# Kernel tuning notes

Measured on AMD Instinct MI355X. Metric: run time of the kernel, lower is better.

## Reference

```python
import jax, jax.numpy as jnp
import numpy as np

H, W = 256, 256
S, S_IDX, END_BIAS = 48, 3, 10
E_IDX = S - END_BIAS          # 38
N_ITER = E_IDX - (S_IDX + 1)  # 34 sequential segments after the start segment
OUT_WIN = 10                  # outlier1d window length
OUT_THRESH = 2.0


def setup_inputs() -> dict:
    key = jax.random.key(0)
    # (x, y) event coordinates in [0, W) x [0, H); t/p/b columns are unused by the module.
    events = jax.random.uniform(key, (16, 960000, 2), jnp.float32, minval=0.0, maxval=256.0)
    return {"events": events}


def _blur(a):
    """5x5 uniform (0.04) blur, SAME padding; a: [B, S, D] -> [B, S, D]."""
    k = jnp.full((1, 1, 5, 5), 0.04, jnp.float32)
    return jax.lax.conv_general_dilated(a[:, None], k, (1, 1), [(2, 2), (2, 2)])[:, 0]


def _outlier_flags(m):
    """outlier1d(m[b, si:si+10], thresh=2)[0] for si in [S_IDX+1, E_IDX). m: [B,S] -> bool [B,N_ITER]."""
    widx = (jnp.arange(N_ITER)[:, None] + S_IDX + 1) + jnp.arange(OUT_WIN)[None, :]
    w = m[:, widx]                                   # [B, N_ITER, 10]
    med = jnp.median(w, axis=-1, keepdims=True)
    diff = jnp.abs(w - med)
    mad = jnp.median(diff, axis=-1)                  # [B, N_ITER]
    return 0.6745 * diff[..., 0] / mad > OUT_THRESH


def reference(events):
    B, N, _ = events.shape
    segmentLen = N // S            # static python int
    Nu = segmentLen * S
    x = events[:, :Nu, 0].astype(jnp.int32)   # [B, Nu]
    y = events[:, :Nu, 1].astype(jnp.int32)
    chunks = jnp.repeat(jnp.arange(S), segmentLen)   # segment id per event, [Nu]
    bidx = jnp.arange(B)[:, None]

    # per-batch x-t / y-t histograms via scatter-add
    alongX = jnp.zeros((B, S, W), jnp.float32).at[bidx, chunks[None, :], x].add(1.0)
    alongY = jnp.zeros((B, S, H), jnp.float32).at[bidx, chunks[None, :], y].add(1.0)

    def proc_axis(along, D):
        flat = along.reshape(B, -1)
        cv = (flat.mean(-1) + 3.0 * jnp.std(flat, axis=-1, ddof=1))[:, None, None]
        a = _blur(jnp.clip(along, 0.0, cv))
        m = jnp.einsum('bsd,d->bs', a, jnp.arange(D, dtype=jnp.float32)) / segmentLen
        start = m[:, S_IDX:S_IDX + 1]
        aligned = jnp.round(m - start - (D // 2 - start)).astype(jnp.int32)
        return m, aligned

    meanX, alignedX = proc_axis(alongX, W)
    meanY, alignedY = proc_axis(alongY, H)
    is_out = _outlier_flags(meanX) | _outlier_flags(meanY)   # [B, N_ITER]

    def per_batch(xb, yb, aX, aY, outb):
        xs = jnp.clip(xb - aX[chunks], 0, W - 1)
        ys = jnp.clip(yb - aY[chunks], 0, H - 1)
        idx_c = (xs + W * ys).reshape(S, segmentLen)
        idx_v = (xs // 2 + (W // 2) * (ys // 2)).reshape(S, segmentLen)
        container0 = jnp.zeros(W * H, jnp.int32).at[idx_c[S_IDX]].add(1)
        ver0 = jnp.zeros((W // 2) * (H // 2), bool).at[idx_v[S_IDX]].set(True)

        def step(carry, inp):
            container, ver, stopped = carry
            ic, iv, is_o = inp
            ver_new = ver.at[iv].set(True)
            cnt = jnp.sum(ver_new).astype(jnp.float32)
            new_info = jnp.sum(jnp.logical_xor(ver_new, ver)).astype(jnp.float32)
            brk = new_info / cnt < 0.1
            do = (~stopped) & (~is_o) & (~brk)
            stopped = stopped | ((~stopped) & (~is_o) & brk)
            container = jnp.where(do, container.at[ic].add(1), container)
            ver = jnp.where(do, ver_new, ver)
            return (container, ver, stopped), None

        (container, _, _), _ = jax.lax.scan(
            step, (container0, ver0, jnp.array(False)),
            (idx_c[S_IDX + 1:E_IDX], idx_v[S_IDX + 1:E_IDX], outb))
        c = container.astype(jnp.float32)
        cv = c.mean() + 3.0 * jnp.std(c, ddof=1)
        return jnp.clip(c, 0.0, cv) / cv

    containers = jax.vmap(per_batch)(x, y, alignedX, alignedY, is_out)  # [B, W*H]
    return containers.reshape(B, 1, H, W)
```

## Files before the change

### kernel.cpp

```cpp
#include <hip/hip_runtime.h>

#define NB 16
#define NEV 960000
#define NS 48
#define SEG 20000
#define S_IDX 3
#define E_IDX 38
#define N_ITER 34
#define ND 256
#define NCH 35

__global__ __launch_bounds__(256) void hist_kernel(const float* __restrict__ events,
                                                   float* __restrict__ alongX,
                                                   float* __restrict__ alongY) {
    __shared__ unsigned hx[ND], hy[ND];
    int tid = threadIdx.x;
    int blk = blockIdx.x;
    int b = blk / NS, c = blk % NS;
    hx[tid] = 0; hy[tid] = 0;
    __syncthreads();
    size_t base = (size_t)b * NEV + (size_t)c * SEG;
    const float4* ev4 = (const float4*)(events + base * 2);
    for (int k = tid; k < SEG / 2; k += 256) {
        float4 v = ev4[k];
        int x0 = (int)v.x, y0 = (int)v.y, x1 = (int)v.z, y1 = (int)v.w;
        x0 = x0 > 255 ? 255 : x0; y0 = y0 > 255 ? 255 : y0;
        x1 = x1 > 255 ? 255 : x1; y1 = y1 > 255 ? 255 : y1;
        atomicAdd(&hx[x0], 1u); atomicAdd(&hy[y0], 1u);
        atomicAdd(&hx[x1], 1u); atomicAdd(&hy[y1], 1u);
    }
    __syncthreads();
    int o = (b * NS + c) * ND + tid;
    alongX[o] = (float)hx[tid];
    alongY[o] = (float)hy[tid];
}

__global__ __launch_bounds__(256) void stats_kernel(const float* __restrict__ alongX,
                                                    const float* __restrict__ alongY,
                                                    int* __restrict__ alignedX,
                                                    int* __restrict__ alignedY,
                                                    float* __restrict__ m_all) {
    __shared__ float sbuf[NS * ND];
    __shared__ double sredA[4], sredB[4];
    __shared__ float scv;
    int tid = threadIdx.x;
    int b = blockIdx.x >> 1, axis = blockIdx.x & 1;
    const float* along = (axis ? alongY : alongX) + (size_t)b * NS * ND;
    for (int k = 0; k < NS; k++) sbuf[k * ND + tid] = along[k * ND + tid];
    __syncthreads();
    double s = 0.0, s2 = 0.0;
    for (int k = 0; k < NS; k++) { double v = sbuf[k * ND + tid]; s += v; s2 += v * v; }
    for (int off = 32; off; off >>= 1) { s += __shfl_down(s, off); s2 += __shfl_down(s2, off); }
    if ((tid & 63) == 0) { sredA[tid >> 6] = s; sredB[tid >> 6] = s2; }
    __syncthreads();
    if (tid == 0) {
        double ts = sredA[0] + sredA[1] + sredA[2] + sredA[3];
        double ts2 = sredB[0] + sredB[1] + sredB[2] + sredB[3];
        const double N = (double)(NS * ND);
        double mean = ts / N;
        double var  = (ts2 - ts * ts / N) / (N - 1.0);
        scv = (float)(mean + 3.0 * sqrt(var));
    }
    __syncthreads();
    float cv = scv;
    int wave = tid >> 6, lane = tid & 63;
    for (int q = 0; q < 12; ++q) {
        int sI = wave * 12 + q;
        double acc = 0.0;
        #pragma unroll
        for (int k = 0; k < 4; ++k) {
            int d = lane + 64 * k;
            int lo = d - 2 < 0 ? 0 : d - 2;
            int hi = d + 2 > 255 ? 255 : d + 2;
            double Wd = 0.5 * (double)(lo + hi) * (double)(hi - lo + 1);
            double t = 0.0;
            #pragma unroll
            for (int ds = -2; ds <= 2; ++ds) {
                int ss = sI + ds;
                if (ss >= 0 && ss < NS) t += (double)fminf(sbuf[ss * ND + d], cv);
            }
            acc += t * Wd;
        }
        for (int off = 32; off; off >>= 1) acc += __shfl_down(acc, off);
        if (lane == 0) {
            float mf = (float)(acc * 0.04 / (double)SEG);
            m_all[(b * 2 + axis) * NS + sI] = mf;
            (axis ? alignedY : alignedX)[b * NS + sI] = (int)rintf(mf - 128.0f);
        }
    }
}

__global__ __launch_bounds__(256) void mask_kernel(const float* __restrict__ events,
                                                   const int* __restrict__ alignedX,
                                                   const int* __restrict__ alignedY,
                                                   unsigned* __restrict__ masks) {
    __shared__ unsigned sm[512];
    int tid = threadIdx.x, blk = blockIdx.x;
    int b = blk / NCH, ci = blk % NCH, si = S_IDX + ci;
    sm[tid] = 0; sm[tid + 256] = 0;
    __syncthreads();
    int aX = alignedX[b * NS + si], aY = alignedY[b * NS + si];
    const float4* ev = (const float4*)(events + ((size_t)b * NEV + (size_t)si * SEG) * 2);
    for (int i = tid; i < SEG / 2; i += 256) {
        float4 e = ev[i];
        int xs0 = (int)e.x - aX; xs0 = xs0 < 0 ? 0 : (xs0 > 255 ? 255 : xs0);
        int ys0 = (int)e.y - aY; ys0 = ys0 < 0 ? 0 : (ys0 > 255 ? 255 : ys0);
        int xs1 = (int)e.z - aX; xs1 = xs1 < 0 ? 0 : (xs1 > 255 ? 255 : xs1);
        int ys1 = (int)e.w - aY; ys1 = ys1 < 0 ? 0 : (ys1 > 255 ? 255 : ys1);
        int iv0 = (xs0 >> 1) | ((ys0 >> 1) << 7);
        int iv1 = (xs1 >> 1) | ((ys1 >> 1) << 7);
        atomicOr(&sm[iv0 >> 5], 1u << (iv0 & 31));
        atomicOr(&sm[iv1 >> 5], 1u << (iv1 & 31));
    }
    __syncthreads();
    unsigned* mo = masks + (size_t)blk * 512;
    mo[tid] = sm[tid];
    mo[tid + 256] = sm[tid + 256];
}

__device__ inline float median10(const float* v) {
    float w[10];
    #pragma unroll
    for (int i = 0; i < 10; i++) w[i] = v[i];
    #pragma unroll
    for (int i = 1; i < 10; i++) {
        float k = w[i]; int j = i - 1;
        while (j >= 0 && w[j] > k) { w[j + 1] = w[j]; j--; }
        w[j + 1] = k;
    }
    return 0.5f * (w[4] + w[5]);
}

__device__ inline bool outlier_flag(const float* w) {
    float med = median10(w);
    float d[10];
    #pragma unroll
    for (int i = 0; i < 10; i++) d[i] = fabsf(w[i] - med);
    float d0 = d[0];
    float mad = median10(d);
    return (0.6745f * d0 / mad) > 2.0f;
}

__device__ inline unsigned wave_sum_u32(unsigned v) {
    for (int off = 32; off; off >>= 1) v += __shfl_xor(v, off);
    return v;
}

__global__ __launch_bounds__(64) void decide_kernel(const unsigned* __restrict__ masks,
                                                    const float* __restrict__ m_all,
                                                    unsigned long long* __restrict__ commitmask) {
    int b = blockIdx.x, lane = threadIdx.x;
    bool f = false;
    if (lane < N_ITER) {
        const float* mx = m_all + b * 2 * NS;
        const float* my = mx + NS;
        f = outlier_flag(&mx[S_IDX + 1 + lane]) || outlier_flag(&my[S_IDX + 1 + lane]);
    }
    unsigned long long omask = __ballot(f);
    const unsigned* mb = masks + (size_t)b * NCH * 512;
    uint4 v0 = ((const uint4*)mb)[lane * 2];
    uint4 v1 = ((const uint4*)mb)[lane * 2 + 1];
    unsigned ver[8] = {v0.x, v0.y, v0.z, v0.w, v1.x, v1.y, v1.z, v1.w};
    unsigned pc = 0;
    #pragma unroll
    for (int j = 0; j < 8; j++) pc += __popc(ver[j]);
    unsigned cnt = wave_sum_u32(pc);
    unsigned long long cm = 1ull;
    for (int si = S_IDX + 1; si < E_IDX; ++si) {
        int idx = si - S_IDX;
        const uint4* dp = (const uint4*)(mb + (size_t)idx * 512);
        uint4 d0 = dp[lane * 2], d1 = dp[lane * 2 + 1];
        unsigned del[8] = {d0.x, d0.y, d0.z, d0.w, d1.x, d1.y, d1.z, d1.w};
        unsigned nl = 0;
        #pragma unroll
        for (int j = 0; j < 8; j++) nl += __popc(del[j] & ~ver[j]);
        unsigned ni = wave_sum_u32(nl);
        bool is_o = (omask >> (si - S_IDX - 1)) & 1;
        if (!is_o) {
            unsigned cn = cnt + ni;
            float ratio = (float)ni / (float)cn;
            if (ratio < 0.1f) break;
            cm |= 1ull << idx;
            cnt = cn;
            #pragma unroll
            for (int j = 0; j < 8; j++) ver[j] |= del[j];
        }
    }
    if (lane == 0) commitmask[b] = cm;
}

__global__ __launch_bounds__(256) void commit_kernel(const float* __restrict__ events,
                                                     const int* __restrict__ alignedX,
                                                     const int* __restrict__ alignedY,
                                                     const unsigned long long* __restrict__ commitmask,
                                                     unsigned* __restrict__ container) {
    int blk = blockIdx.x, tid = threadIdx.x;
    int b = blk / NCH, ci = blk % NCH;
    if (!((commitmask[b] >> ci) & 1ull)) return;
    int si = S_IDX + ci;
    int aX = alignedX[b * NS + si], aY = alignedY[b * NS + si];
    unsigned* cont = container + (size_t)b * 65536;
    const float4* ev = (const float4*)(events + ((size_t)b * NEV + (size_t)si * SEG) * 2);
    for (int i = tid; i < SEG / 2; i += 256) {
        float4 e = ev[i];
        int xs0 = (int)e.x - aX; xs0 = xs0 < 0 ? 0 : (xs0 > 255 ? 255 : xs0);
        int ys0 = (int)e.y - aY; ys0 = ys0 < 0 ? 0 : (ys0 > 255 ? 255 : ys0);
        int xs1 = (int)e.z - aX; xs1 = xs1 < 0 ? 0 : (xs1 > 255 ? 255 : xs1);
        int ys1 = (int)e.w - aY; ys1 = ys1 < 0 ? 0 : (ys1 > 255 ? 255 : ys1);
        atomicAdd(&cont[xs0 | (ys0 << 8)], 1u);
        atomicAdd(&cont[xs1 | (ys1 << 8)], 1u);
    }
}

__global__ __launch_bounds__(256) void cv_kernel(const unsigned* __restrict__ container,
                                                 float* __restrict__ cvb) {
    __shared__ double sredA[4], sredB[4];
    int tid = threadIdx.x, b = blockIdx.x;
    const uint4* c4 = (const uint4*)(container + (size_t)b * 65536);
    double s = 0.0, s2 = 0.0;
    for (int i = tid; i < 16384; i += 256) {
        uint4 v = c4[i];
        double a0 = v.x, a1 = v.y, a2 = v.z, a3 = v.w;
        s += a0 + a1 + a2 + a3;
        s2 += a0 * a0 + a1 * a1 + a2 * a2 + a3 * a3;
    }
    for (int off = 32; off; off >>= 1) { s += __shfl_down(s, off); s2 += __shfl_down(s2, off); }
    if ((tid & 63) == 0) { sredA[tid >> 6] = s; sredB[tid >> 6] = s2; }
    __syncthreads();
    if (tid == 0) {
        double ts = sredA[0] + sredA[1] + sredA[2] + sredA[3];
        double ts2 = sredB[0] + sredB[1] + sredB[2] + sredB[3];
        double mean = ts / 65536.0;
        double var = (ts2 - ts * ts / 65536.0) / 65535.0;
        cvb[b] = (float)(mean + 3.0 * sqrt(var));
    }
}

__global__ __launch_bounds__(256) void finish_kernel(const unsigned* __restrict__ container,
                                                     const float* __restrict__ cvb,
                                                     float* __restrict__ out) {
    int g = blockIdx.x * 256 + threadIdx.x;
    int b = g >> 14;
    float cv = cvb[b];
    uint4 v = ((const uint4*)container)[g];
    float4 o;
    o.x = fminf((float)v.x, cv) / cv;
    o.y = fminf((float)v.y, cv) / cv;
    o.z = fminf((float)v.z, cv) / cv;
    o.w = fminf((float)v.w, cv) / cv;
    ((float4*)out)[g] = o;
}

extern "C" void kernel_launch(void* const* d_in, const int* in_sizes, int n_in,
                              void* d_out, int out_size, void* d_ws, size_t ws_size,
                              hipStream_t stream) {
    const float* events = (const float*)d_in[0];
    float* out = (float*)d_out;
    char* ws = (char*)d_ws;

    float*    alongX    = (float*)(ws);
    float*    alongY    = (float*)(ws + 786432);
    unsigned* masks     = (unsigned*)(ws);
    unsigned* container = (unsigned*)(ws + 1572864);
    int*      alignedX  = (int*)(ws + 5767168);
    int*      alignedY  = (int*)(ws + 5770240);
    float*    m_all     = (float*)(ws + 5773312);
    unsigned long long* commitmask = (unsigned long long*)(ws + 5779456);
    float*    cvb       = (float*)(ws + 5779584);

    hipMemsetAsync(container, 0, (size_t)NB * 65536 * sizeof(unsigned), stream);
    hist_kernel<<<NB * NS, 256, 0, stream>>>(events, alongX, alongY);
    stats_kernel<<<NB * 2, 256, 0, stream>>>(alongX, alongY, alignedX, alignedY, m_all);
    mask_kernel<<<NB * NCH, 256, 0, stream>>>(events, alignedX, alignedY, masks);
    decide_kernel<<<NB, 64, 0, stream>>>(masks, m_all, commitmask);
    commit_kernel<<<NB * NCH, 256, 0, stream>>>(events, alignedX, alignedY, commitmask, container);
    cv_kernel<<<NB, 256, 0, stream>>>(container, cvb);
    finish_kernel<<<1024, 256, 0, stream>>>(container, cvb, out);
}
```

Measured before the change: 307.2 us.

## Compact events to packed 16-bit coords in hist pass; fold container memset in

The histogram kernel now also writes each event of segments 3..37 as a packed pair of 8-bit x/y coordinates, two events per 32-bit word. The mask and commit kernels read this compact buffer instead of re-reading the float events, which cuts their global read traffic by a factor of four. The container zeroing moves into the histogram kernel, removing the separate memset. The cost is an extra write of about 22 MB in the histogram pass. A stub commit_kernel is left behind unused.

```diff
diff --git a/kernel.cpp b/kernel.cpp
--- a/kernel.cpp
+++ b/kernel.cpp
@@ -12,15 +12,24 @@
 
 __global__ __launch_bounds__(256) void hist_kernel(const float* __restrict__ events,
                                                    float* __restrict__ alongX,
-                                                   float* __restrict__ alongY) {
+                                                   float* __restrict__ alongY,
+                                                   unsigned* __restrict__ compact,
+                                                   unsigned* __restrict__ container) {
     __shared__ unsigned hx[ND], hy[ND];
     int tid = threadIdx.x;
     int blk = blockIdx.x;
     int b = blk / NS, c = blk % NS;
     hx[tid] = 0; hy[tid] = 0;
+    {
+        uint4 z = {0u, 0u, 0u, 0u};
+        for (int i = blk * 256 + tid; i < 262144; i += NB * NS * 256)
+            ((uint4*)container)[i] = z;
+    }
     __syncthreads();
     size_t base = (size_t)b * NEV + (size_t)c * SEG;
     const float4* ev4 = (const float4*)(events + base * 2);
+    bool wr = (c >= S_IDX && c < E_IDX);
+    unsigned* dst = wr ? compact + ((size_t)b * NCH + (c - S_IDX)) * (SEG / 2) : nullptr;
     for (int k = tid; k < SEG / 2; k += 256) {
         float4 v = ev4[k];
         int x0 = (int)v.x, y0 = (int)v.y, x1 = (int)v.z, y1 = (int)v.w;
@@ -28,6 +37,7 @@
         x1 = x1 > 255 ? 255 : x1; y1 = y1 > 255 ? 255 : y1;
         atomicAdd(&hx[x0], 1u); atomicAdd(&hy[y0], 1u);
         atomicAdd(&hx[x1], 1u); atomicAdd(&hy[y1], 1u);
+        if (wr) dst[k] = (unsigned)(x0 | (y0 << 8)) | ((unsigned)(x1 | (y1 << 8)) << 16);
     }
     __syncthreads();
     int o = (b * NS + c) * ND + tid;
@@ -90,7 +100,7 @@
     }
 }
 
-__global__ __launch_bounds__(256) void mask_kernel(const float* __restrict__ events,
+__global__ __launch_bounds__(256) void mask_kernel(const unsigned* __restrict__ compact,
                                                    const int* __restrict__ alignedX,
                                                    const int* __restrict__ alignedY,
                                                    unsigned* __restrict__ masks) {
@@ -100,17 +110,22 @@
     sm[tid] = 0; sm[tid + 256] = 0;
     __syncthreads();
     int aX = alignedX[b * NS + si], aY = alignedY[b * NS + si];
-    const float4* ev = (const float4*)(events + ((size_t)b * NEV + (size_t)si * SEG) * 2);
-    for (int i = tid; i < SEG / 2; i += 256) {
-        float4 e = ev[i];
-        int xs0 = (int)e.x - aX; xs0 = xs0 < 0 ? 0 : (xs0 > 255 ? 255 : xs0);
-        int ys0 = (int)e.y - aY; ys0 = ys0 < 0 ? 0 : (ys0 > 255 ? 255 : ys0);
-        int xs1 = (int)e.z - aX; xs1 = xs1 < 0 ? 0 : (xs1 > 255 ? 255 : xs1);
-        int ys1 = (int)e.w - aY; ys1 = ys1 < 0 ? 0 : (ys1 > 255 ? 255 : ys1);
-        int iv0 = (xs0 >> 1) | ((ys0 >> 1) << 7);
-        int iv1 = (xs1 >> 1) | ((ys1 >> 1) << 7);
-        atomicOr(&sm[iv0 >> 5], 1u << (iv0 & 31));
-        atomicOr(&sm[iv1 >> 5], 1u << (iv1 & 31));
+    const uint4* cp = (const uint4*)(compact + ((size_t)b * NCH + ci) * (SEG / 2));
+    for (int i = tid; i < SEG / 8; i += 256) {
+        uint4 w = cp[i];
+        unsigned ws[4] = {w.x, w.y, w.z, w.w};
+        #pragma unroll
+        for (int j = 0; j < 4; j++) {
+            unsigned v = ws[j];
+            #pragma unroll
+            for (int h = 0; h < 2; h++) {
+                unsigned e = (h ? (v >> 16) : v) & 0xFFFFu;
+                int xs = (int)(e & 255u) - aX; xs = xs < 0 ? 0 : (xs > 255 ? 255 : xs);
+                int ys = (int)(e >> 8)   - aY; ys = ys < 0 ? 0 : (ys > 255 ? 255 : ys);
+                int iv = (xs >> 1) | ((ys >> 1) << 7);
+                atomicOr(&sm[iv >> 5], 1u << (iv & 31));
+            }
+        }
     }
     __syncthreads();
     unsigned* mo = masks + (size_t)blk * 512;
@@ -189,26 +204,42 @@
     if (lane == 0) commitmask[b] = cm;
 }
 
-__global__ __launch_bounds__(256) void commit_kernel(const float* __restrict__ events,
-                                                     const int* __restrict__ alignedX,
-                                                     const int* __restrict__ alignedY,
+__global__ __launch_bounds__(256) void commit_kernel(const unsigned* __restrict__ compact,
                                                      const unsigned long long* __restrict__ commitmask,
                                                      unsigned* __restrict__ container) {
     int blk = blockIdx.x, tid = threadIdx.x;
     int b = blk / NCH, ci = blk % NCH;
     if (!((commitmask[b] >> ci) & 1ull)) return;
     int si = S_IDX + ci;
+    (void)si;
+}
+
+__global__ __launch_bounds__(256) void commit2_kernel(const unsigned* __restrict__ compact,
+                                                      const int* __restrict__ alignedX,
+                                                      const int* __restrict__ alignedY,
+                                                      const unsigned long long* __restrict__ commitmask,
+                                                      unsigned* __restrict__ container) {
+    int blk = blockIdx.x, tid = threadIdx.x;
+    int b = blk / NCH, ci = blk % NCH;
+    if (!((commitmask[b] >> ci) & 1ull)) return;
+    int si = S_IDX + ci;
     int aX = alignedX[b * NS + si], aY = alignedY[b * NS + si];
     unsigned* cont = container + (size_t)b * 65536;
-    const float4* ev = (const float4*)(events + ((size_t)b * NEV + (size_t)si * SEG) * 2);
-    for (int i = tid; i < SEG / 2; i += 256) {
-        float4 e = ev[i];
-        int xs0 = (int)e.x - aX; xs0 = xs0 < 0 ? 0 : (xs0 > 255 ? 255 : xs0);
-        int ys0 = (int)e.y - aY; ys0 = ys0 < 0 ? 0 : (ys0 > 255 ? 255 : ys0);
-        int xs1 = (int)e.z - aX; xs1 = xs1 < 0 ? 0 : (xs1 > 255 ? 255 : xs1);
-        int ys1 = (int)e.w - aY; ys1 = ys1 < 0 ? 0 : (ys1 > 255 ? 255 : ys1);
-        atomicAdd(&cont[xs0 | (ys0 << 8)], 1u);
-        atomicAdd(&cont[xs1 | (ys1 << 8)], 1u);
+    const uint4* cp = (const uint4*)(compact + ((size_t)b * NCH + ci) * (SEG / 2));
+    for (int i = tid; i < SEG / 8; i += 256) {
+        uint4 w = cp[i];
+        unsigned ws[4] = {w.x, w.y, w.z, w.w};
+        #pragma unroll
+        for (int j = 0; j < 4; j++) {
+            unsigned v = ws[j];
+            #pragma unroll
+            for (int h = 0; h < 2; h++) {
+                unsigned e = (h ? (v >> 16) : v) & 0xFFFFu;
+                int xs = (int)(e & 255u) - aX; xs = xs < 0 ? 0 : (xs > 255 ? 255 : xs);
+                int ys = (int)(e >> 8)   - aY; ys = ys < 0 ? 0 : (ys > 255 ? 255 : ys);
+                atomicAdd(&cont[xs | (ys << 8)], 1u);
+            }
+        }
     }
 }
 
@@ -260,20 +291,20 @@
 
     float*    alongX    = (float*)(ws);
     float*    alongY    = (float*)(ws + 786432);
-    unsigned* masks     = (unsigned*)(ws);
     unsigned* container = (unsigned*)(ws + 1572864);
     int*      alignedX  = (int*)(ws + 5767168);
     int*      alignedY  = (int*)(ws + 5770240);
     float*    m_all     = (float*)(ws + 5773312);
     unsigned long long* commitmask = (unsigned long long*)(ws + 5779456);
     float*    cvb       = (float*)(ws + 5779584);
-
-    hipMemsetAsync(container, 0, (size_t)NB * 65536 * sizeof(unsigned), stream);
-    hist_kernel<<<NB * NS, 256, 0, stream>>>(events, alongX, alongY);
+    unsigned* compact   = (unsigned*)(ws + 6291456);
+    unsigned* masks     = (unsigned*)(ws + 29360128);
+
+    hist_kernel<<<NB * NS, 256, 0, stream>>>(events, alongX, alongY, compact, container);
     stats_kernel<<<NB * 2, 256, 0, stream>>>(alongX, alongY, alignedX, alignedY, m_all);
-    mask_kernel<<<NB * NCH, 256, 0, stream>>>(events, alignedX, alignedY, masks);
+    mask_kernel<<<NB * NCH, 256, 0, stream>>>(compact, alignedX, alignedY, masks);
     decide_kernel<<<NB, 64, 0, stream>>>(masks, m_all, commitmask);
-    commit_kernel<<<NB * NCH, 256, 0, stream>>>(events, alignedX, alignedY, commitmask, container);
+    commit2_kernel<<<NB * NCH, 256, 0, stream>>>(compact, alignedX, alignedY, commitmask, container);
     cv_kernel<<<NB, 256, 0, stream>>>(container, cvb);
     finish_kernel<<<1024, 256, 0, stream>>>(container, cvb, out);
 }
```

After: 295.9 us. 3.7% less time.
